# Performance work log

Hardware: AMD Instinct MI355X
Metric: run time of the kernel (lower is better)

Reference implementation:

```python
import jax, jax.numpy as jnp
import numpy as np

SEQ_LEN = 2048
NUM_GLOBAL = 32
NEG_INF = float('-inf')


def _build_mask(seq_len=SEQ_LEN, num_global=NUM_GLOBAL):
    # Causal mask: triu(ones).T == lower-triangular ones; zeros -> -inf, ones -> 0.
    m = np.where(np.tril(np.ones((seq_len, seq_len), dtype=np.float32)) == 1.0, 0.0, NEG_INF)
    # Deterministic 'random.sample' of global tokens (fixed for reproducibility).
    rng = np.random.default_rng(0)
    gtok = rng.choice(seq_len, size=num_global, replace=False)
    m[:, gtok] = 0.0
    m[gtok, :] = 0.0
    return jnp.asarray(m)


def setup_inputs() -> dict:
    key = jax.random.key(0)
    ks = jax.random.split(key, 9)
    B, S, D_IN, D_QK = 8, SEQ_LEN, 1024, 128
    return {
        'q': jax.random.normal(ks[0], (B, S, D_IN), dtype=jnp.float32),
        'k': jax.random.normal(ks[1], (B, S, D_IN), dtype=jnp.float32),
        'v': jax.random.normal(ks[2], (B, S, D_IN), dtype=jnp.float32),
        'Wq': jax.random.normal(ks[3], (D_QK, D_IN), dtype=jnp.float32) * 0.02,
        'bq': jax.random.normal(ks[4], (D_QK,), dtype=jnp.float32) * 0.02,
        'Wk': jax.random.normal(ks[5], (D_QK, D_IN), dtype=jnp.float32) * 0.02,
        'bk': jax.random.normal(ks[6], (D_QK,), dtype=jnp.float32) * 0.02,
        'Wv': jax.random.normal(ks[7], (D_QK, D_IN), dtype=jnp.float32) * 0.02,
        'bv': jax.random.normal(ks[8], (D_QK,), dtype=jnp.float32) * 0.02,
    }


def reference(q, k, v, Wq, bq, Wk, bk, Wv, bv):
    # Linear projections (torch nn.Linear: x @ W.T + b)
    Q = jnp.einsum('bsd,qd->bsq', q, Wq) + bq   # [B,S,dq]
    K = jnp.einsum('bsd,qd->bsq', k, Wk) + bk   # [B,S,dk]
    V = jnp.einsum('bsd,qd->bsq', v, Wv) + bv   # [B,S,dk]
    mask = _build_mask()                        # [S,S] static causal+global
    scale = K.shape[-1] ** 0.5
    scores = jnp.einsum('bqd,bkd->bqk', Q, K)   # dense QK^T [B,S,S]
    scores = (scores + mask) / scale            # (-inf stays -inf)
    attn = jax.nn.softmax(scores, axis=-1)
    return jnp.einsum('bqk,bkd->bqd', attn, V)
```

## Files before the change

### kernel.cpp

```cpp
#include <hip/hip_runtime.h>
#include <cstdint>

constexpr int SEQ  = 2048;
constexpr int DIN  = 1024;
constexpr int DQK  = 128;
constexpr int NB   = 8;
constexpr int MTOT = NB * SEQ;
constexpr float INV_SCALE = 0.08838834764831845f;

typedef __attribute__((ext_vector_type(8))) short  short8;
typedef __attribute__((ext_vector_type(4))) float  floatx4;
typedef __attribute__((ext_vector_type(4))) int    intx4;

struct GM { unsigned long long w[32]; };

static void compute_gtok(unsigned long long bits[32]) {
  typedef unsigned __int128 u128;
  uint32_t pool[4];
  uint32_t hc = 0x43b0d7e5u;
  auto hashmix = [&hc](uint32_t v) -> uint32_t {
    v ^= hc; hc *= 0x931e8875u; v *= hc; v ^= v >> 16; return v;
  };
  auto mixf = [](uint32_t x, uint32_t y) -> uint32_t {
    uint32_t r = x * 0xca01f9ddu - y * 0x4973f715u;
    r ^= r >> 16; return r;
  };
  pool[0] = hashmix(0u);
  for (int i = 1; i < 4; ++i) pool[i] = hashmix(0u);
  for (int s = 0; s < 4; ++s)
    for (int d = 0; d < 4; ++d)
      if (s != d) pool[d] = mixf(pool[d], hashmix(pool[s]));
  uint32_t hb = 0x8b51f9ddu;
  uint32_t st[8];
  for (int i = 0; i < 8; ++i) {
    uint32_t dv = pool[i & 3];
    dv ^= hb; hb *= 0x58f38dedu; dv *= hb; dv ^= dv >> 16;
    st[i] = dv;
  }
  uint64_t sv[4];
  for (int i = 0; i < 4; ++i)
    sv[i] = (uint64_t)st[2 * i] | ((uint64_t)st[2 * i + 1] << 32);
  const u128 MUL = ((u128)2549297995355413924ULL << 64) | (u128)4865540595714422341ULL;
  u128 initstate = ((u128)sv[0] << 64) | sv[1];
  u128 initseq   = ((u128)sv[2] << 64) | sv[3];
  u128 state = 0;
  u128 inc = (initseq << 1) | 1;
  state = state * MUL + inc;
  state += initstate;
  state = state * MUL + inc;
  bool has32 = false; uint32_t cache32 = 0;
  auto next64 = [&]() -> uint64_t {
    state = state * MUL + inc;
    uint64_t hi = (uint64_t)(state >> 64);
    uint64_t lo = (uint64_t)state;
    unsigned rot = (unsigned)(state >> 122);
    uint64_t x = hi ^ lo;
    return (x >> rot) | (x << ((64u - rot) & 63u));
  };
  auto next32 = [&]() -> uint32_t {
    if (has32) { has32 = false; return cache32; }
    uint64_t n = next64();
    has32 = true; cache32 = (uint32_t)(n >> 32);
    return (uint32_t)n;
  };
  bool in_set[SEQ];
  for (int i = 0; i < SEQ; ++i) in_set[i] = false;
  for (uint32_t j = 2016; j < 2048; ++j) {
    uint32_t rng_excl = j + 1;
    uint64_t m = (uint64_t)next32() * rng_excl;
    uint32_t leftover = (uint32_t)m;
    if (leftover < rng_excl) {
      uint32_t threshold = (0xFFFFFFFFu - j) % rng_excl;
      while (leftover < threshold) {
        m = (uint64_t)next32() * rng_excl;
        leftover = (uint32_t)m;
      }
    }
    uint32_t val = (uint32_t)(m >> 32);
    if (in_set[val]) in_set[j] = true;
    else in_set[val] = true;
  }
  for (int i = 0; i < 32; ++i) bits[i] = 0ULL;
  for (int t = 0; t < SEQ; ++t)
    if (in_set[t]) bits[t >> 6] |= (1ULL << (t & 63));
}

__device__ __forceinline__ void ldsld16(const void* g, void* l) {
  __builtin_amdgcn_global_load_lds(
      (const __attribute__((address_space(1))) unsigned int*)g,
      (__attribute__((address_space(3))) unsigned int*)l, 16, 0, 0);
}
__device__ __forceinline__ bool gbit(const GM& g, int j) {
  return (g.w[j >> 6] >> (j & 63)) & 1ULL;
}
__device__ __forceinline__ void split4(float4 x, unsigned hw[2], unsigned lw[2]) {
  unsigned u0 = __float_as_uint(x.x), u1 = __float_as_uint(x.y);
  unsigned u2 = __float_as_uint(x.z), u3 = __float_as_uint(x.w);
  hw[0] = __builtin_amdgcn_perm(u1, u0, 0x07060302u);
  hw[1] = __builtin_amdgcn_perm(u3, u2, 0x07060302u);
  unsigned r0 = __float_as_uint(x.x - __uint_as_float(u0 & 0xFFFF0000u));
  unsigned r1 = __float_as_uint(x.y - __uint_as_float(u1 & 0xFFFF0000u));
  unsigned r2 = __float_as_uint(x.z - __uint_as_float(u2 & 0xFFFF0000u));
  unsigned r3 = __float_as_uint(x.w - __uint_as_float(u3 & 0xFFFF0000u));
  lw[0] = __builtin_amdgcn_perm(r1, r0, 0x07060302u);
  lw[1] = __builtin_amdgcn_perm(r3, r2, 0x07060302u);
}
__device__ __forceinline__ void split1(float v, unsigned short& h, unsigned short& l) {
  unsigned u = __float_as_uint(v);
  h = (unsigned short)(u >> 16);
  float rr = v - __uint_as_float(u & 0xFFFF0000u);
  l = (unsigned short)(__float_as_uint(rr) >> 16);
}
__device__ __forceinline__ unsigned short bfr_rne(float v) {
  unsigned u = __float_as_uint(v);
  return (unsigned short)((u + 0x7FFFu + ((u >> 16) & 1u)) >> 16);
}

__global__ __launch_bounds__(256) void wconv_kernel(
    const float* __restrict__ Wq, const float* __restrict__ Wk, const float* __restrict__ Wv,
    unsigned short* __restrict__ Whi, unsigned short* __restrict__ Wlo) {
  const float* W = blockIdx.y == 0 ? Wq : blockIdx.y == 1 ? Wk : Wv;
  size_t base = (size_t)blockIdx.y * DQK * DIN;
  int e = (blockIdx.x * 256 + threadIdx.x) * 4;
  float4 x = *(const float4*)&W[e];
  unsigned hw[2], lw[2];
  split4(x, hw, lw);
  *(uint2*)&Whi[base + e] = make_uint2(hw[0], hw[1]);
  *(uint2*)&Wlo[base + e] = make_uint2(lw[0], lw[1]);
}

__global__ __launch_bounds__(256, 3) void proj_kernel(
    const float* __restrict__ xq, const float* __restrict__ xk, const float* __restrict__ xv,
    const unsigned short* __restrict__ Whi, const unsigned short* __restrict__ Wlo,
    const float* __restrict__ bq, const float* __restrict__ bk, const float* __restrict__ bv,
    unsigned short* __restrict__ Qb, unsigned short* __restrict__ Kb,
    unsigned short* __restrict__ Vth) {
  const int which = blockIdx.y;
  const float* X    = which == 0 ? xq : which == 1 ? xk : xv;
  const float* bias = which == 0 ? bq : which == 1 ? bk : bv;
  const int m0 = blockIdx.x * 64;

  __shared__ unsigned short Xh[64 * 64];
  __shared__ unsigned short Xl[64 * 64];
  __shared__ unsigned short Wh[128 * 64];
  __shared__ unsigned short Wl[128 * 64];

  const int tid = threadIdx.x;
  const int w = tid >> 6, lane = tid & 63, l15 = lane & 15, quad = lane >> 4;
  const int mh = (w >> 1) * 32, nh = (w & 1) * 64;

  floatx4 acc[2][4] = {};
  float biasv[4];
#pragma unroll
  for (int j = 0; j < 4; ++j) biasv[j] = bias[nh + j * 16 + l15];

  const unsigned short* WhiP = Whi + (size_t)which * DQK * DIN;
  const unsigned short* WloP = Wlo + (size_t)which * DQK * DIN;

  for (int kb = 0; kb < DIN; kb += 64) {
    __syncthreads();
#pragma unroll
    for (int i = 0; i < 4; ++i) {
      int f = tid + i * 256;
      int r = f >> 4, c4 = f & 15;
      float4 x = *(const float4*)&X[(size_t)(m0 + r) * DIN + kb + c4 * 4];
      unsigned hw[2], lw[2];
      split4(x, hw, lw);
      int off = r * 64 + (((c4 >> 1) ^ (r & 7)) * 8) + (c4 & 1) * 4;
      *(uint2*)&Xh[off] = make_uint2(hw[0], hw[1]);
      *(uint2*)&Xl[off] = make_uint2(lw[0], lw[1]);
    }
#pragma unroll
    for (int i = 0; i < 8; ++i) {
      int c = w * 8 + i;
      int plane = c >> 4, cc = c & 15;
      int F = cc * 1024 + lane * 16;
      int n = F >> 7, gs = (F >> 4) & 7, gl = gs ^ (n & 7);
      const unsigned short* gp = (plane ? WloP : WhiP) + (size_t)n * DIN + kb + gl * 8;
      ldsld16(gp, (char*)(plane ? Wl : Wh) + cc * 1024);
    }
    __syncthreads();
#pragma unroll
    for (int ks = 0; ks < 2; ++ks) {
      short8 Ah[2], Al[2], Bh[4], Bl[4];
#pragma unroll
      for (int ms = 0; ms < 2; ++ms) {
        int off = (mh + ms * 16 + l15) * 64 + (((ks * 4 + quad) ^ (l15 & 7)) * 8);
        Ah[ms] = *(const short8*)&Xh[off];
        Al[ms] = *(const short8*)&Xl[off];
      }
#pragma unroll
      for (int ns = 0; ns < 4; ++ns) {
        int off = (nh + ns * 16 + l15) * 64 + (((ks * 4 + quad) ^ (l15 & 7)) * 8);
        Bh[ns] = *(const short8*)&Wh[off];
        Bl[ns] = *(const short8*)&Wl[off];
      }
#pragma unroll
      for (int i = 0; i < 2; ++i)
#pragma unroll
        for (int j = 0; j < 4; ++j) {
          floatx4 c = acc[i][j];
          c = __builtin_amdgcn_mfma_f32_16x16x32_bf16(Ah[i], Bh[j], c, 0, 0, 0);
          c = __builtin_amdgcn_mfma_f32_16x16x32_bf16(Ah[i], Bl[j], c, 0, 0, 0);
          c = __builtin_amdgcn_mfma_f32_16x16x32_bf16(Al[i], Bh[j], c, 0, 0, 0);
          acc[i][j] = c;
        }
    }
  }

  if (which < 2) {
    unsigned short* O = which == 0 ? Qb : Kb;
#pragma unroll
    for (int i = 0; i < 2; ++i)
#pragma unroll
      for (int j = 0; j < 4; ++j)
#pragma unroll
        for (int r = 0; r < 4; ++r) {
          int m = mh + i * 16 + quad * 4 + r;
          int n = nh + j * 16 + l15;
          O[(size_t)(m0 + m) * DQK + n] = bfr_rne(acc[i][j][r] + biasv[j]);
        }
  } else {
    __syncthreads();
    unsigned short* VH = Wh;
#pragma unroll
    for (int i = 0; i < 2; ++i)
#pragma unroll
      for (int j = 0; j < 4; ++j)
#pragma unroll
        for (int r = 0; r < 4; ++r) {
          int s = mh + i * 16 + quad * 4 + r;
          int d = nh + j * 16 + l15;
          VH[d * 64 + (((s >> 3) ^ (d & 7)) * 8) + (s & 7)] =
              bfr_rne(acc[i][j][r] + biasv[j]);
        }
    __syncthreads();
    int b = m0 >> 11, s0 = m0 & 2047;
#pragma unroll
    for (int i = 0; i < 4; ++i) {
      int cch = i * 256 + tid;
      int d = cch >> 3, gI = cch & 7;
      int loff = d * 64 + ((gI ^ (d & 7)) * 8);
      intx4 vh = *(const intx4*)&VH[loff];
      *(intx4*)&Vth[((size_t)b * DQK + d) * SEQ + s0 + gI * 8] = vh;
    }
  }
}

__global__ __launch_bounds__(256, 3) void attn_kernel(
    const unsigned short* __restrict__ Qb, const unsigned short* __restrict__ Kb,
    const unsigned short* __restrict__ Vth,
    float* __restrict__ Opart, float2* __restrict__ ML, GM g, unsigned int t64) {
  __shared__ unsigned short Ks[64 * 128];
  __shared__ unsigned short Vh[128 * 64];
  __shared__ unsigned short Ph[4][16 * 72];
  __shared__ unsigned short Pl[4][16 * 72];

  const int tid = threadIdx.x;
  const int w = tid >> 6, lane = tid & 63, l15 = lane & 15, quad = lane >> 4;
  const int b = blockIdx.y;
  const int qt = blockIdx.x / 3, s3 = blockIdx.x - qt * 3;
  const int qs = qt * 64;

  short8 qf[4];
  const unsigned short* Qrow = Qb + ((size_t)(b * SEQ + qs + w * 16 + l15)) * DQK;
#pragma unroll
  for (int j = 0; j < 4; ++j) qf[j] = *(const short8*)&Qrow[j * 32 + quad * 8];

  int rowi[4]; bool growb[4];
#pragma unroll
  for (int r = 0; r < 4; ++r) {
    rowi[r] = qs + w * 16 + quad * 4 + r;
    growb[r] = gbit(g, rowi[r]);
  }

  floatx4 o[8] = {};
  float m_r[4] = {-1e30f, -1e30f, -1e30f, -1e30f};
  float l_r[4] = {0.f, 0.f, 0.f, 0.f};

  const bool qhasg = (t64 >> qt) & 1;
  const unsigned short* KbB = Kb  + (size_t)b * SEQ * DQK;
  const unsigned short* VhB = Vth + (size_t)b * DQK * SEQ;

  for (int kt = s3; kt < 32; kt += 3) {
    const int ks0 = kt * 64;
    if (!((ks0 <= qs + 63) || ((t64 >> kt) & 1) || qhasg)) continue;

    __syncthreads();
#pragma unroll
    for (int i = 0; i < 8; ++i) {
      int c = w * 8 + i;
      if (c < 16) {
        int F = c * 1024 + lane * 16;
        int r = F >> 8, gs = (F >> 4) & 15, gl = gs ^ (r & 15);
        ldsld16(KbB + (size_t)(ks0 + r) * DQK + gl * 8, (char*)Ks + c * 1024);
      } else {
        int cc = c - 16;
        int F = cc * 1024 + lane * 16;
        int d = F >> 7, gs = (F >> 4) & 7, gl = gs ^ (d & 7);
        ldsld16(VhB + (size_t)d * SEQ + ks0 + gl * 8, (char*)Vh + cc * 1024);
      }
    }
    __syncthreads();

    floatx4 S[4];
#pragma unroll
    for (int c4 = 0; c4 < 4; ++c4) {
      floatx4 s = {0.f, 0.f, 0.f, 0.f};
#pragma unroll
      for (int j = 0; j < 4; ++j) {
        short8 kf = *(const short8*)&Ks[(c4 * 16 + l15) * 128 + (((j * 4 + quad) ^ l15) * 8)];
        s = __builtin_amdgcn_mfma_f32_16x16x32_bf16(qf[j], kf, s, 0, 0, 0);
      }
      S[c4] = s;
    }

    float z[4][4];
    float mx[4] = {-1e30f, -1e30f, -1e30f, -1e30f};
#pragma unroll
    for (int c4 = 0; c4 < 4; ++c4) {
      int col = ks0 + c4 * 16 + l15;
      bool cg = gbit(g, col);
#pragma unroll
      for (int r = 0; r < 4; ++r) {
        bool ok = (col <= rowi[r]) || cg || growb[r];
        float zz = ok ? S[c4][r] * INV_SCALE : -1e30f;
        z[c4][r] = zz;
        mx[r] = fmaxf(mx[r], zz);
      }
    }
#pragma unroll
    for (int d = 1; d < 16; d <<= 1)
#pragma unroll
      for (int r = 0; r < 4; ++r) mx[r] = fmaxf(mx[r], __shfl_xor(mx[r], d));
    float alpha[4], rs[4] = {0.f, 0.f, 0.f, 0.f};
#pragma unroll
    for (int r = 0; r < 4; ++r) {
      float mn = fmaxf(m_r[r], mx[r]);
      alpha[r] = __expf(m_r[r] - mn);
      m_r[r] = mn;
    }
    float p[4][4];
#pragma unroll
    for (int c4 = 0; c4 < 4; ++c4)
#pragma unroll
      for (int r = 0; r < 4; ++r) {
        float pp = __expf(z[c4][r] - m_r[r]);
        p[c4][r] = pp;
        rs[r] += pp;
      }
#pragma unroll
    for (int d = 1; d < 16; d <<= 1)
#pragma unroll
      for (int r = 0; r < 4; ++r) rs[r] += __shfl_xor(rs[r], d);
#pragma unroll
    for (int r = 0; r < 4; ++r) l_r[r] = l_r[r] * alpha[r] + rs[r];
#pragma unroll
    for (int n = 0; n < 8; ++n)
#pragma unroll
      for (int r = 0; r < 4; ++r) o[n][r] *= alpha[r];

#pragma unroll
    for (int c4 = 0; c4 < 4; ++c4)
#pragma unroll
      for (int r = 0; r < 4; ++r) {
        unsigned short h, lo;
        split1(p[c4][r], h, lo);
        int off = (quad * 4 + r) * 72 + c4 * 16 + l15;
        Ph[w][off] = h; Pl[w][off] = lo;
      }
    short8 pf[2], pg[2];
#pragma unroll
    for (int kq = 0; kq < 2; ++kq) {
      int off = l15 * 72 + kq * 32 + quad * 8;
      pf[kq] = *(const short8*)&Ph[w][off];
      pg[kq] = *(const short8*)&Pl[w][off];
    }

#pragma unroll
    for (int n = 0; n < 8; ++n) {
      int drow = n * 16 + l15;
#pragma unroll
      for (int kq = 0; kq < 2; ++kq) {
        int off = drow * 64 + (((kq * 4 + quad) ^ (drow & 7)) * 8);
        short8 vhf = *(const short8*)&Vh[off];
        floatx4 c = o[n];
        c = __builtin_amdgcn_mfma_f32_16x16x32_bf16(pf[kq], vhf, c, 0, 0, 0);
        c = __builtin_amdgcn_mfma_f32_16x16x32_bf16(pg[kq], vhf, c, 0, 0, 0);
        o[n] = c;
      }
    }
  }

  const size_t grp = (size_t)(b * 32 + qt) * 3 + s3;
  float* Op = Opart + grp * 64 * 128;
#pragma unroll
  for (int n = 0; n < 8; ++n)
#pragma unroll
    for (int r = 0; r < 4; ++r)
      Op[(w * 16 + quad * 4 + r) * 128 + n * 16 + l15] = o[n][r];
  if (l15 == 0) {
#pragma unroll
    for (int r = 0; r < 4; ++r)
      ML[grp * 64 + w * 16 + quad * 4 + r] = make_float2(m_r[r], l_r[r]);
  }
}

__global__ __launch_bounds__(256) void merge_kernel(
    const float* __restrict__ Opart, const float2* __restrict__ ML,
    float* __restrict__ Out) {
  const int t = threadIdx.x;
  const int row = blockIdx.x * 2 + (t >> 7);
  const int col = t & 127;
  const int grp = row >> 6;
  const int rin = row & 63;
  const size_t base = (size_t)grp * 3;
  float2 ml0 = ML[(base + 0) * 64 + rin];
  float2 ml1 = ML[(base + 1) * 64 + rin];
  float2 ml2 = ML[(base + 2) * 64 + rin];
  const float m = fmaxf(fmaxf(ml0.x, ml1.x), ml2.x);
  const float w0 = __expf(ml0.x - m), w1 = __expf(ml1.x - m), w2 = __expf(ml2.x - m);
  const float denom = w0 * ml0.y + w1 * ml1.y + w2 * ml2.y;
  const float o0 = Opart[((base + 0) * 64 + rin) * 128 + col];
  const float o1 = Opart[((base + 1) * 64 + rin) * 128 + col];
  const float o2 = Opart[((base + 2) * 64 + rin) * 128 + col];
  Out[(size_t)row * 128 + col] = (w0 * o0 + w1 * o1 + w2 * o2) / denom;
}

extern "C" void kernel_launch(void* const* d_in, const int* in_sizes, int n_in,
                              void* d_out, int out_size, void* d_ws, size_t ws_size,
                              hipStream_t stream) {
  const float* q  = (const float*)d_in[0];
  const float* k  = (const float*)d_in[1];
  const float* v  = (const float*)d_in[2];
  const float* Wq = (const float*)d_in[3];
  const float* bq = (const float*)d_in[4];
  const float* Wk = (const float*)d_in[5];
  const float* bk = (const float*)d_in[6];
  const float* Wv = (const float*)d_in[7];
  const float* bv = (const float*)d_in[8];
  float* out = (float*)d_out;

  unsigned short* Qb  = (unsigned short*)d_ws;
  unsigned short* Kb2 = Qb  + (size_t)MTOT * DQK;
  unsigned short* Vth = Kb2 + (size_t)MTOT * DQK;
  unsigned short* Whi = Vth + (size_t)MTOT * DQK;
  unsigned short* Wlo = Whi + (size_t)3 * DQK * DIN;
  float*  Opart = (float*)(Wlo + (size_t)3 * DQK * DIN);
  float2* ML    = (float2*)(Opart + (size_t)3 * MTOT * DQK);

  GM g;
  compute_gtok(g.w);
  unsigned int t64 = 0;
  for (int t = 0; t < 32; ++t) if (g.w[t] != 0ULL) t64 |= (1u << t);

  hipLaunchKernelGGL(wconv_kernel, dim3(128, 3), dim3(256), 0, stream,
                     Wq, Wk, Wv, Whi, Wlo);
  hipLaunchKernelGGL(proj_kernel, dim3(256, 3), dim3(256), 0, stream,
                     q, k, v, Whi, Wlo, bq, bk, bv, Qb, Kb2, Vth);
  hipLaunchKernelGGL(attn_kernel, dim3(96, 8), dim3(256), 0, stream,
                     Qb, Kb2, Vth, Opart, ML, g, t64);
  hipLaunchKernelGGL(merge_kernel, dim3(MTOT / 2), dim3(256), 0, stream,
                     Opart, ML, out);
}
```

Before: 280.2 us.

## Register-prefetch next K-slice of X and W in projection GEMM

The projection GEMM now loads the next 64-wide K slice of X and the split W planes into registers while the current slice is computed. It replaces the direct global-to-LDS loads of W with register staging and a manual waitcnt plus barrier. The goal is to hide global memory latency behind the MFMA work. In exchange it uses more VGPRs (12 vector registers of prefetch data plus precomputed pointers), which may reduce occupancy.

```diff
diff --git a/kernel.cpp b/kernel.cpp
--- a/kernel.cpp
+++ b/kernel.cpp
@@ -157,29 +157,53 @@
   const unsigned short* WhiP = Whi + (size_t)which * DQK * DIN;
   const unsigned short* WloP = Wlo + (size_t)which * DQK * DIN;
 
+  const float* xsrc[4];
+  int xoff[4];
+#pragma unroll
+  for (int i = 0; i < 4; ++i) {
+    int f = tid + i * 256;
+    int r = f >> 4, c4 = f & 15;
+    xsrc[i] = &X[(size_t)(m0 + r) * DIN + c4 * 4];
+    xoff[i] = r * 64 + (((c4 >> 1) ^ (r & 7)) * 8) + (c4 & 1) * 4;
+  }
+  const unsigned short* wsrc[8];
+  unsigned short* wdst[8];
+#pragma unroll
+  for (int i = 0; i < 8; ++i) {
+    int c = w * 8 + i;
+    int plane = c >> 4, cc = c & 15;
+    int F = cc * 1024 + lane * 16;
+    int n = F >> 7, gs = (F >> 4) & 7, gl = gs ^ (n & 7);
+    wsrc[i] = (plane ? WloP : WhiP) + (size_t)n * DIN + gl * 8;
+    wdst[i] = (unsigned short*)((char*)(plane ? Wl : Wh) + cc * 1024) + lane * 8;
+  }
+
+  float4 xr[4];
+  intx4  wr[8];
+#pragma unroll
+  for (int i = 0; i < 4; ++i) xr[i] = *(const float4*)xsrc[i];
+#pragma unroll
+  for (int i = 0; i < 8; ++i) wr[i] = *(const intx4*)wsrc[i];
+
   for (int kb = 0; kb < DIN; kb += 64) {
     __syncthreads();
 #pragma unroll
     for (int i = 0; i < 4; ++i) {
-      int f = tid + i * 256;
-      int r = f >> 4, c4 = f & 15;
-      float4 x = *(const float4*)&X[(size_t)(m0 + r) * DIN + kb + c4 * 4];
       unsigned hw[2], lw[2];
-      split4(x, hw, lw);
-      int off = r * 64 + (((c4 >> 1) ^ (r & 7)) * 8) + (c4 & 1) * 4;
-      *(uint2*)&Xh[off] = make_uint2(hw[0], hw[1]);
-      *(uint2*)&Xl[off] = make_uint2(lw[0], lw[1]);
-    }
-#pragma unroll
-    for (int i = 0; i < 8; ++i) {
-      int c = w * 8 + i;
-      int plane = c >> 4, cc = c & 15;
-      int F = cc * 1024 + lane * 16;
-      int n = F >> 7, gs = (F >> 4) & 7, gl = gs ^ (n & 7);
-      const unsigned short* gp = (plane ? WloP : WhiP) + (size_t)n * DIN + kb + gl * 8;
-      ldsld16(gp, (char*)(plane ? Wl : Wh) + cc * 1024);
-    }
-    __syncthreads();
+      split4(xr[i], hw, lw);
+      *(uint2*)&Xh[xoff[i]] = make_uint2(hw[0], hw[1]);
+      *(uint2*)&Xl[xoff[i]] = make_uint2(lw[0], lw[1]);
+    }
+#pragma unroll
+    for (int i = 0; i < 8; ++i) *(intx4*)wdst[i] = wr[i];
+    if (kb + 64 < DIN) {
+#pragma unroll
+      for (int i = 0; i < 4; ++i) xr[i] = *(const float4*)(xsrc[i] + kb + 64);
+#pragma unroll
+      for (int i = 0; i < 8; ++i) wr[i] = *(const intx4*)(wsrc[i] + kb + 64);
+    }
+    asm volatile("s_waitcnt lgkmcnt(0)" ::: "memory");
+    __builtin_amdgcn_s_barrier();
 #pragma unroll
     for (int ks = 0; ks < 2; ++ks) {
       short8 Ah[2], Al[2], Bh[4], Bl[4];
```

Result: slower. 289.3 us (+3.3%).

## Double-buffer projection K-loop with async LDS loads and split fp32 in registers

Applied to the files above, without the earlier changes.

The projection GEMM K-loop now loads raw fp32 X tiles and the bf16 hi/lo weight tiles straight into LDS with async direct-to-LDS loads. It uses two buffers with K-step 32, so the next tile is fetched while the current one is multiplied. The fp32-to-bf16 hi/lo split of X moves from the global-load stage to register time after the LDS read. This removes one barrier per iteration and aims to hide global-load latency. In exchange the block uses 48KB of LDS, which may reduce occupancy at 3 blocks per CU, and the split work is repeated for each MFMA fragment read.

```diff
diff --git a/kernel.cpp b/kernel.cpp
--- a/kernel.cpp
+++ b/kernel.cpp
@@ -140,10 +140,7 @@
   const float* bias = which == 0 ? bq : which == 1 ? bk : bv;
   const int m0 = blockIdx.x * 64;
 
-  __shared__ unsigned short Xh[64 * 64];
-  __shared__ unsigned short Xl[64 * 64];
-  __shared__ unsigned short Wh[128 * 64];
-  __shared__ unsigned short Wl[128 * 64];
+  __shared__ __align__(16) unsigned char LDSb[49152];
 
   const int tid = threadIdx.x;
   const int w = tid >> 6, lane = tid & 63, l15 = lane & 15, quad = lane >> 4;
@@ -157,55 +154,82 @@
   const unsigned short* WhiP = Whi + (size_t)which * DQK * DIN;
   const unsigned short* WloP = Wlo + (size_t)which * DQK * DIN;
 
-  for (int kb = 0; kb < DIN; kb += 64) {
+  const char* gp[6];
+  unsigned    ldsoff[6];
+#pragma unroll
+  for (int i = 0; i < 6; ++i) {
+    if (i < 2) {
+      int cx = w + 4 * i;
+      int R  = cx * 8 + (lane >> 3);
+      int sg = (lane & 7) ^ (R & 7);
+      gp[i] = (const char*)(X + (size_t)(m0 + R) * DIN + sg * 4);
+      ldsoff[i] = cx * 1024;
+    } else {
+      int ii = (i < 4) ? i - 2 : i - 4;
+      int cw = w + 4 * ii;
+      int n  = cw * 16 + (lane >> 2);
+      int sg = (lane & 3) ^ (n & 3);
+      const unsigned short* Wp = (i < 4) ? WhiP : WloP;
+      gp[i] = (const char*)(Wp + (size_t)n * DIN + sg * 8);
+      ldsoff[i] = ((i < 4) ? 16384u : 32768u) + cw * 1024;
+    }
+  }
+
+  auto stage = [&](int nb) {
+#pragma unroll
+    for (int i = 0; i < 6; ++i) {
+      ldsld16(gp[i], LDSb + ldsoff[i] + nb * 8192);
+      gp[i] += (i < 2) ? 128 : 64;
+    }
+  };
+
+  int buf = 0;
+  stage(0);
+  __syncthreads();
+
+  for (int it = 0; it < 32; ++it) {
+    if (it + 1 < 32) stage(buf ^ 1);
+
+    const float*          Xs  = (const float*)(LDSb + buf * 8192);
+    const unsigned short* WhS = (const unsigned short*)(LDSb + 16384 + buf * 8192);
+    const unsigned short* WlS = (const unsigned short*)(LDSb + 32768 + buf * 8192);
+
+    short8 Ah[2], Al[2];
+#pragma unroll
+    for (int ms = 0; ms < 2; ++ms) {
+      int R = mh + ms * 16 + l15;
+      const float* row = Xs + R * 32;
+      float4 xa = *(const float4*)&row[((2 * quad) ^ (R & 7)) * 4];
+      float4 xb = *(const float4*)&row[((2 * quad + 1) ^ (R & 7)) * 4];
+      unsigned ha[2], la[2], hb2[2], lb2[2];
+      split4(xa, ha, la);
+      split4(xb, hb2, lb2);
+      union { short8 v; unsigned u[4]; } H, L;
+      H.u[0] = ha[0]; H.u[1] = ha[1]; H.u[2] = hb2[0]; H.u[3] = hb2[1];
+      L.u[0] = la[0]; L.u[1] = la[1]; L.u[2] = lb2[0]; L.u[3] = lb2[1];
+      Ah[ms] = H.v; Al[ms] = L.v;
+    }
+    short8 Bh[4], Bl[4];
+#pragma unroll
+    for (int ns = 0; ns < 4; ++ns) {
+      int n = nh + ns * 16 + l15;
+      int off = n * 32 + ((quad ^ (n & 3)) * 8);
+      Bh[ns] = *(const short8*)&WhS[off];
+      Bl[ns] = *(const short8*)&WlS[off];
+    }
+#pragma unroll
+    for (int i = 0; i < 2; ++i)
+#pragma unroll
+      for (int j = 0; j < 4; ++j) {
+        floatx4 c = acc[i][j];
+        c = __builtin_amdgcn_mfma_f32_16x16x32_bf16(Ah[i], Bh[j], c, 0, 0, 0);
+        c = __builtin_amdgcn_mfma_f32_16x16x32_bf16(Ah[i], Bl[j], c, 0, 0, 0);
+        c = __builtin_amdgcn_mfma_f32_16x16x32_bf16(Al[i], Bh[j], c, 0, 0, 0);
+        acc[i][j] = c;
+      }
+
     __syncthreads();
-#pragma unroll
-    for (int i = 0; i < 4; ++i) {
-      int f = tid + i * 256;
-      int r = f >> 4, c4 = f & 15;
-      float4 x = *(const float4*)&X[(size_t)(m0 + r) * DIN + kb + c4 * 4];
-      unsigned hw[2], lw[2];
-      split4(x, hw, lw);
-      int off = r * 64 + (((c4 >> 1) ^ (r & 7)) * 8) + (c4 & 1) * 4;
-      *(uint2*)&Xh[off] = make_uint2(hw[0], hw[1]);
-      *(uint2*)&Xl[off] = make_uint2(lw[0], lw[1]);
-    }
-#pragma unroll
-    for (int i = 0; i < 8; ++i) {
-      int c = w * 8 + i;
-      int plane = c >> 4, cc = c & 15;
-      int F = cc * 1024 + lane * 16;
-      int n = F >> 7, gs = (F >> 4) & 7, gl = gs ^ (n & 7);
-      const unsigned short* gp = (plane ? WloP : WhiP) + (size_t)n * DIN + kb + gl * 8;
-      ldsld16(gp, (char*)(plane ? Wl : Wh) + cc * 1024);
-    }
-    __syncthreads();
-#pragma unroll
-    for (int ks = 0; ks < 2; ++ks) {
-      short8 Ah[2], Al[2], Bh[4], Bl[4];
-#pragma unroll
-      for (int ms = 0; ms < 2; ++ms) {
-        int off = (mh + ms * 16 + l15) * 64 + (((ks * 4 + quad) ^ (l15 & 7)) * 8);
-        Ah[ms] = *(const short8*)&Xh[off];
-        Al[ms] = *(const short8*)&Xl[off];
-      }
-#pragma unroll
-      for (int ns = 0; ns < 4; ++ns) {
-        int off = (nh + ns * 16 + l15) * 64 + (((ks * 4 + quad) ^ (l15 & 7)) * 8);
-        Bh[ns] = *(const short8*)&Wh[off];
-        Bl[ns] = *(const short8*)&Wl[off];
-      }
-#pragma unroll
-      for (int i = 0; i < 2; ++i)
-#pragma unroll
-        for (int j = 0; j < 4; ++j) {
-          floatx4 c = acc[i][j];
-          c = __builtin_amdgcn_mfma_f32_16x16x32_bf16(Ah[i], Bh[j], c, 0, 0, 0);
-          c = __builtin_amdgcn_mfma_f32_16x16x32_bf16(Ah[i], Bl[j], c, 0, 0, 0);
-          c = __builtin_amdgcn_mfma_f32_16x16x32_bf16(Al[i], Bh[j], c, 0, 0, 0);
-          acc[i][j] = c;
-        }
-    }
+    buf ^= 1;
   }
 
   if (which < 2) {
@@ -222,7 +246,7 @@
         }
   } else {
     __syncthreads();
-    unsigned short* VH = Wh;
+    unsigned short* VH = (unsigned short*)LDSb;
 #pragma unroll
     for (int i = 0; i < 2; ++i)
 #pragma unroll
```

Result: slower. 290.0 us (+3.5%).

## Double-buffer weight tiles and stream X directly into registers in projection

Applied to the files above, without the earlier changes.

Rewrites the projection GEMM so each wave owns 16 rows and all 128 output columns. The X operand is loaded from global straight into registers and split into bf16 hi/lo fragments, with no trip through LDS. Weight tiles are double-buffered in a 64KB LDS region and prefetched one k-step ahead, with explicit waitcnt and barriers. This is meant to overlap global loads with MFMA work and remove X staging and one barrier per step, at the cost of more LDS per block and lower occupancy (launch bounds reduced from 3 to 2).

```diff
diff --git a/kernel.cpp b/kernel.cpp
--- a/kernel.cpp
+++ b/kernel.cpp
@@ -129,7 +129,59 @@
   *(uint2*)&Wlo[base + e] = make_uint2(lw[0], lw[1]);
 }
 
-__global__ __launch_bounds__(256, 3) void proj_kernel(
+#define PROJ_ITER(IT, XC)                                                      \
+  {                                                                            \
+    const int it_ = (IT);                                                      \
+    asm volatile("s_waitcnt vmcnt(4) lgkmcnt(0)" ::: "memory");                \
+    __builtin_amdgcn_s_barrier();                                              \
+    const int kb_ = it_ * 64;                                                  \
+    if (it_ + 1 < 16) {                                                        \
+      const unsigned nb_ = ((unsigned)(it_ + 1) & 1u) * 32768u;                \
+      _Pragma("unroll")                                                        \
+      for (int i = 0; i < 8; ++i)                                              \
+        ldsld16(wsrc[i] + kb_ + 64, wdst[i] + nb_);                            \
+    }                                                                          \
+    short8 Ah[2], Al[2];                                                       \
+    _Pragma("unroll")                                                          \
+    for (int ks = 0; ks < 2; ++ks) {                                           \
+      unsigned ha[2], la[2], hb[2], lb[2];                                     \
+      split4(XC[2 * ks], ha, la);                                              \
+      split4(XC[2 * ks + 1], hb, lb);                                          \
+      union { short8 v; unsigned u[4]; } H, L;                                 \
+      H.u[0] = ha[0]; H.u[1] = ha[1]; H.u[2] = hb[0]; H.u[3] = hb[1];          \
+      L.u[0] = la[0]; L.u[1] = la[1]; L.u[2] = lb[0]; L.u[3] = lb[1];          \
+      Ah[ks] = H.v; Al[ks] = L.v;                                              \
+    }                                                                          \
+    __builtin_amdgcn_sched_barrier(0);                                         \
+    if (it_ + 1 < 16) {                                                        \
+      const int kb2_ = (it_ + 2 < 16) ? kb_ + 128 : 0;                         \
+      XC[0] = *(const float4*)(xp + kb2_ + 0);                                 \
+      XC[1] = *(const float4*)(xp + kb2_ + 4);                                 \
+      XC[2] = *(const float4*)(xp + kb2_ + 32);                                \
+      XC[3] = *(const float4*)(xp + kb2_ + 36);                                \
+    }                                                                          \
+    __builtin_amdgcn_sched_barrier(0);                                         \
+    const unsigned short* WhS_ =                                               \
+        (const unsigned short*)(LDSb + ((unsigned)it_ & 1u) * 32768u);         \
+    const unsigned short* WlS_ =                                               \
+        (const unsigned short*)(LDSb + ((unsigned)it_ & 1u) * 32768u + 16384u);\
+    _Pragma("unroll")                                                          \
+    for (int ks = 0; ks < 2; ++ks)                                             \
+      _Pragma("unroll")                                                        \
+      for (int nj = 0; nj < 8; ++nj) {                                         \
+        int n_ = nj * 16 + l15;                                                \
+        int off_ = n_ * 64 + (((ks * 4 + quad) ^ (n_ & 7)) * 8);               \
+        short8 bh = *(const short8*)&WhS_[off_];                               \
+        short8 bl = *(const short8*)&WlS_[off_];                               \
+        floatx4 c = acc[nj];                                                   \
+        c = __builtin_amdgcn_mfma_f32_16x16x32_bf16(Ah[ks], bh, c, 0, 0, 0);   \
+        c = __builtin_amdgcn_mfma_f32_16x16x32_bf16(Ah[ks], bl, c, 0, 0, 0);   \
+        c = __builtin_amdgcn_mfma_f32_16x16x32_bf16(Al[ks], bh, c, 0, 0, 0);   \
+        acc[nj] = c;                                                           \
+      }                                                                        \
+  }
+
+__global__ __launch_bounds__(256, 2) void proj_kernel(
     const float* __restrict__ xq, const float* __restrict__ xk, const float* __restrict__ xv,
     const unsigned short* __restrict__ Whi, const unsigned short* __restrict__ Wlo,
     const float* __restrict__ bq, const float* __restrict__ bk, const float* __restrict__ bv,
@@ -140,100 +192,72 @@
   const float* bias = which == 0 ? bq : which == 1 ? bk : bv;
   const int m0 = blockIdx.x * 64;
 
-  __shared__ unsigned short Xh[64 * 64];
-  __shared__ unsigned short Xl[64 * 64];
-  __shared__ unsigned short Wh[128 * 64];
-  __shared__ unsigned short Wl[128 * 64];
+  __shared__ __align__(16) unsigned char LDSb[65536];
 
   const int tid = threadIdx.x;
   const int w = tid >> 6, lane = tid & 63, l15 = lane & 15, quad = lane >> 4;
-  const int mh = (w >> 1) * 32, nh = (w & 1) * 64;
-
-  floatx4 acc[2][4] = {};
-  float biasv[4];
-#pragma unroll
-  for (int j = 0; j < 4; ++j) biasv[j] = bias[nh + j * 16 + l15];
+
+  floatx4 acc[8] = {};
 
   const unsigned short* WhiP = Whi + (size_t)which * DQK * DIN;
   const unsigned short* WloP = Wlo + (size_t)which * DQK * DIN;
 
-  for (int kb = 0; kb < DIN; kb += 64) {
-    __syncthreads();
-#pragma unroll
-    for (int i = 0; i < 4; ++i) {
-      int f = tid + i * 256;
-      int r = f >> 4, c4 = f & 15;
-      float4 x = *(const float4*)&X[(size_t)(m0 + r) * DIN + kb + c4 * 4];
-      unsigned hw[2], lw[2];
-      split4(x, hw, lw);
-      int off = r * 64 + (((c4 >> 1) ^ (r & 7)) * 8) + (c4 & 1) * 4;
-      *(uint2*)&Xh[off] = make_uint2(hw[0], hw[1]);
-      *(uint2*)&Xl[off] = make_uint2(lw[0], lw[1]);
-    }
-#pragma unroll
-    for (int i = 0; i < 8; ++i) {
-      int c = w * 8 + i;
-      int plane = c >> 4, cc = c & 15;
-      int F = cc * 1024 + lane * 16;
-      int n = F >> 7, gs = (F >> 4) & 7, gl = gs ^ (n & 7);
-      const unsigned short* gp = (plane ? WloP : WhiP) + (size_t)n * DIN + kb + gl * 8;
-      ldsld16(gp, (char*)(plane ? Wl : Wh) + cc * 1024);
-    }
-    __syncthreads();
-#pragma unroll
-    for (int ks = 0; ks < 2; ++ks) {
-      short8 Ah[2], Al[2], Bh[4], Bl[4];
-#pragma unroll
-      for (int ms = 0; ms < 2; ++ms) {
-        int off = (mh + ms * 16 + l15) * 64 + (((ks * 4 + quad) ^ (l15 & 7)) * 8);
-        Ah[ms] = *(const short8*)&Xh[off];
-        Al[ms] = *(const short8*)&Xl[off];
-      }
-#pragma unroll
-      for (int ns = 0; ns < 4; ++ns) {
-        int off = (nh + ns * 16 + l15) * 64 + (((ks * 4 + quad) ^ (l15 & 7)) * 8);
-        Bh[ns] = *(const short8*)&Wh[off];
-        Bl[ns] = *(const short8*)&Wl[off];
-      }
-#pragma unroll
-      for (int i = 0; i < 2; ++i)
-#pragma unroll
-        for (int j = 0; j < 4; ++j) {
-          floatx4 c = acc[i][j];
-          c = __builtin_amdgcn_mfma_f32_16x16x32_bf16(Ah[i], Bh[j], c, 0, 0, 0);
-          c = __builtin_amdgcn_mfma_f32_16x16x32_bf16(Ah[i], Bl[j], c, 0, 0, 0);
-          c = __builtin_amdgcn_mfma_f32_16x16x32_bf16(Al[i], Bh[j], c, 0, 0, 0);
-          acc[i][j] = c;
-        }
-    }
+  const unsigned short* wsrc[8];
+  unsigned char* wdst[8];
+#pragma unroll
+  for (int i = 0; i < 8; ++i) {
+    int c = w * 8 + i;
+    int plane = c >> 4, cc = c & 15;
+    int n = cc * 8 + (lane >> 3);
+    int gl = (lane & 7) ^ (n & 7);
+    wsrc[i] = (plane ? WloP : WhiP) + (size_t)n * DIN + gl * 8;
+    wdst[i] = LDSb + plane * 16384 + cc * 1024;
+  }
+
+  const float* xp = X + (size_t)(m0 + w * 16 + l15) * DIN + quad * 8;
+
+#pragma unroll
+  for (int i = 0; i < 8; ++i) ldsld16(wsrc[i], wdst[i]);
+  float4 xrA[4], xrB[4];
+  xrA[0] = *(const float4*)(xp + 0);
+  xrA[1] = *(const float4*)(xp + 4);
+  xrA[2] = *(const float4*)(xp + 32);
+  xrA[3] = *(const float4*)(xp + 36);
+  xrB[0] = *(const float4*)(xp + 64);
+  xrB[1] = *(const float4*)(xp + 68);
+  xrB[2] = *(const float4*)(xp + 96);
+  xrB[3] = *(const float4*)(xp + 100);
+
+  for (int it2 = 0; it2 < 16; it2 += 2) {
+    PROJ_ITER(it2, xrA);
+    PROJ_ITER(it2 + 1, xrB);
   }
 
   if (which < 2) {
     unsigned short* O = which == 0 ? Qb : Kb;
 #pragma unroll
-    for (int i = 0; i < 2; ++i)
-#pragma unroll
-      for (int j = 0; j < 4; ++j)
-#pragma unroll
-        for (int r = 0; r < 4; ++r) {
-          int m = mh + i * 16 + quad * 4 + r;
-          int n = nh + j * 16 + l15;
-          O[(size_t)(m0 + m) * DQK + n] = bfr_rne(acc[i][j][r] + biasv[j]);
-        }
+    for (int nj = 0; nj < 8; ++nj) {
+      float bv = bias[nj * 16 + l15];
+#pragma unroll
+      for (int r = 0; r < 4; ++r) {
+        int m = w * 16 + quad * 4 + r;
+        O[(size_t)(m0 + m) * DQK + nj * 16 + l15] = bfr_rne(acc[nj][r] + bv);
+      }
+    }
   } else {
     __syncthreads();
-    unsigned short* VH = Wh;
-#pragma unroll
-    for (int i = 0; i < 2; ++i)
-#pragma unroll
-      for (int j = 0; j < 4; ++j)
-#pragma unroll
-        for (int r = 0; r < 4; ++r) {
-          int s = mh + i * 16 + quad * 4 + r;
-          int d = nh + j * 16 + l15;
-          VH[d * 64 + (((s >> 3) ^ (d & 7)) * 8) + (s & 7)] =
-              bfr_rne(acc[i][j][r] + biasv[j]);
-        }
+    unsigned short* VH = (unsigned short*)LDSb;
+#pragma unroll
+    for (int nj = 0; nj < 8; ++nj) {
+      float bv = bias[nj * 16 + l15];
+#pragma unroll
+      for (int r = 0; r < 4; ++r) {
+        int s = w * 16 + quad * 4 + r;
+        int d = nj * 16 + l15;
+        VH[d * 64 + (((s >> 3) ^ (d & 7)) * 8) + (s & 7)] =
+            bfr_rne(acc[nj][r] + bv);
+      }
+    }
     __syncthreads();
     int b = m0 >> 11, s0 = m0 & 2047;
 #pragma unroll
```

Result: slower. 295.2 us (+5.4%).
